# Kernel tuning notes

Measured on AMD Instinct MI355X. Metric: run time of the kernel, lower is better.

## Reference

```python
import jax, jax.numpy as jnp
import numpy as np

HEIGHT = 32
SIGMA = 2.0
NUM_NEGATIVE = 4096
N, C = 32, 512
L = HEIGHT * HEIGHT


def _grid_weight(height: int, sigma: float) -> jnp.ndarray:
    # distance_weights: pairwise Euclidean distance between grid points
    ii, jj = np.meshgrid(np.arange(height), np.arange(height), indexing='ij')
    coords = np.stack([ii.ravel(), jj.ravel()], axis=1).astype(np.float32)  # [L, 2]
    d2 = ((coords[:, None, :] - coords[None, :, :]) ** 2).sum(-1)  # squared dist [L, L]
    w = -(0.5 / sigma ** 2) * d2
    np.fill_diagonal(w, -np.inf)
    return jax.nn.softmax(jnp.asarray(w, dtype=jnp.float32), axis=1)


def setup_inputs() -> dict:
    key = jax.random.key(0)
    k1, k2 = jax.random.split(key)
    embedding = jax.random.normal(k1, (N, L, C), dtype=jnp.float32)
    weight = _grid_weight(HEIGHT, SIGMA)  # [L, L] softmax-normalized grid kernel
    neg_indices = jax.random.randint(k2, (NUM_NEGATIVE,), 0, N * L, dtype=jnp.int64)
    return {"embedding": embedding, "weight": weight, "neg_indices": neg_indices}


def reference(embedding, weight, neg_indices):
    n, l, c = embedding.shape
    # F.normalize(dim=-1), eps=1e-12
    norm = jnp.maximum(jnp.linalg.norm(embedding, axis=-1, keepdims=True), 1e-12)
    e = embedding / norm  # [N, L, C]
    # target = weight @ e  (broadcast over batch)
    target = jnp.einsum('kl,nlc->nkc', weight, e)  # [N, L, C]
    sim_pos = jnp.sum(e * target, axis=-1)  # [N, L]
    flat = e.reshape(-1, c)  # [N*L, C]
    negatives = flat[neg_indices]  # [M, C]
    sim_neg = jnp.einsum('nlc,mc->nlm', e, negatives)  # [N, L, M]
    logits = jnp.concatenate([sim_pos[..., None], sim_neg], axis=2).reshape(n * l, 1 + neg_indices.shape[0])
    # CrossEntropyLoss with target class 0, mean reduction
    loss = -jnp.mean(jax.nn.log_softmax(logits, axis=-1)[:, 0])
    return loss
```

## Files before the change

kernel.cpp:

```cpp
#include <hip/hip_runtime.h>
#include <hip/hip_bf16.h>
#include <stdint.h>

#define L_DIM 1024
#define C_DIM 512
#define CB4 256
#define N_BATCH 32
#define M_NEG 4096
#define NROWS (N_BATCH * L_DIM)

typedef float f32x4 __attribute__((ext_vector_type(4)));
typedef int i32x4 __attribute__((ext_vector_type(4)));
typedef int i32x8 __attribute__((ext_vector_type(8)));

#define E4_SCALE 32.0f
#define MX_SCALE 122
#define FMT_FP4 4

template <int GOFF>
__device__ __forceinline__ void gl_lds16(const uint8_t* g, uint8_t* l) {
  __builtin_amdgcn_global_load_lds(
      (const __attribute__((address_space(1))) void*)g,
      (__attribute__((address_space(3))) void*)l, 16, GOFF, 0);
}

__device__ __forceinline__ uint32_t fp4_enc(float x) {
  const uint32_t s = (__float_as_uint(x) >> 31) << 3;
  const float a = fabsf(x);
  uint32_t c;
  c = a < 0.25f ? 0u
    : a < 0.75f ? 1u
    : a < 1.25f ? 2u
    : a < 1.75f ? 3u
    : a < 2.5f  ? 4u
    : a < 3.5f  ? 5u
    : a < 5.0f  ? 6u : 7u;
  return s | c;
}

__device__ __forceinline__ i32x8 fp4_op(i32x4 d) {
  return __builtin_shufflevector(d, d, 0, 1, 2, 3, -1, -1, -1, -1);
}

__device__ __forceinline__ int swz(int row) { return (row >> 1) & 3; }

#define WAITK(n) asm volatile("s_waitcnt vmcnt(" #n ")\n\ts_barrier" ::: "memory")
#define BARRIER() asm volatile("s_barrier" ::: "memory")

__global__ __launch_bounds__(256) void k_normalize(const float* __restrict__ emb,
                                                   uint8_t* __restrict__ out,
                                                   float* __restrict__ zerobuf,
                                                   float* __restrict__ loss_out) {
  if (blockIdx.x < 256) zerobuf[blockIdx.x * 256 + threadIdx.x] = 0.0f;
  if (blockIdx.x == 0 && threadIdx.x == 0) loss_out[0] = 0.0f;
  const int lane = threadIdx.x & 63;
  const int wave = threadIdx.x >> 6;
  const long row = (long)blockIdx.x * 4 + wave;
  const float4* src = (const float4*)(emb + row * C_DIM);
  float4 v0 = src[2 * lane];
  float4 v1 = src[2 * lane + 1];
  float ss = v0.x * v0.x + v0.y * v0.y + v0.z * v0.z + v0.w * v0.w +
             v1.x * v1.x + v1.y * v1.y + v1.z * v1.z + v1.w * v1.w;
#pragma unroll
  for (int off = 1; off < 64; off <<= 1) ss += __shfl_xor(ss, off, 64);
  const float s = E4_SCALE / fmaxf(sqrtf(ss), 1e-12f);
  uint32_t pk = fp4_enc(v0.x * s)        | (fp4_enc(v0.y * s) << 4) |
                (fp4_enc(v0.z * s) << 8) | (fp4_enc(v0.w * s) << 12) |
                (fp4_enc(v1.x * s) << 16)| (fp4_enc(v1.y * s) << 20) |
                (fp4_enc(v1.z * s) << 24)| (fp4_enc(v1.w * s) << 28);
  ((uint32_t*)(out + row * CB4))[lane] = pk;
}

__global__ __launch_bounds__(256, 4) void k_gemm_fused(
    const uint8_t* __restrict__ E4, const int* __restrict__ idx,
    const float* __restrict__ W, float* __restrict__ rowsum,
    float* __restrict__ simpos) {
  __shared__ __align__(16) unsigned char smem_raw[32768];
  uint8_t* sA = (uint8_t*)smem_raw;
  uint8_t* sB = sA + 16384;

  const int tid = threadIdx.x;
  const int lane = tid & 63;
  const int wave = tid >> 6;
  const int wm = wave >> 1, wn = wave & 1;
  const int q = lane >> 4, c16 = lane & 15;

  const int bid = blockIdx.x;
  const bool is0 = bid >= 2048;
  long rowBase, colBase, n = 0;
  if (is0) {
    const int t = bid - 2048;
    const int xcd = t & 7, slot = t >> 3;
    rowBase = (long)(xcd * 32 + (slot & 31)) * 128;
    colBase = (long)(slot >> 5) * 128;
  } else {
    const int xcd = bid & 7, slot = bid >> 3;
    n = xcd * 4 + (slot & 3);
    const int inner = slot >> 2;
    rowBase = (long)(inner & 7) * 128;
    colBase = (long)(inner >> 3) * 128;
  }
  const long aBase = is0 ? rowBase : n * L_DIM + rowBase;

  const uint8_t* pA[2];
  const uint8_t* pB[2];
#pragma unroll
  for (int r = 0; r < 2; ++r) {
    const int c = r * 256 + tid;
    const int rw = c >> 2, cb = c & 3;
    pA[r] = E4 + (aBase + rw) * CB4 + (cb ^ swz(rw)) * 16;
    const long bRow = is0 ? (long)idx[colBase + rw] : n * L_DIM + colBase + rw;
    pB[r] = E4 + bRow * CB4 + (cb ^ swz(rw)) * 16;
  }

  int ldsB[4], ldsA[4];
#pragma unroll
  for (int j = 0; j < 4; ++j) {
    const int rowB = wn * 64 + j * 16 + c16;
    ldsB[j] = rowB * 64 + (q ^ swz(rowB)) * 16;
    const int rowA = wm * 64 + j * 16 + c16;
    ldsA[j] = rowA * 64 + (q ^ swz(rowA)) * 16;
  }

  f32x4 acc[4][4] = {};

  auto kcompute = [&](int kofs) {
    i32x8 bfr[4];
#pragma unroll
    for (int j = 0; j < 4; ++j)
      bfr[j] = fp4_op(*(const i32x4*)(sB + kofs + ldsB[j]));
#pragma unroll
    for (int i = 0; i < 4; ++i) {
      i32x8 af = fp4_op(*(const i32x4*)(sA + kofs + ldsA[i]));
#pragma unroll
      for (int j = 0; j < 4; ++j)
        acc[i][j] = __builtin_amdgcn_mfma_scale_f32_16x16x128_f8f6f4(
            af, bfr[j], acc[i][j], FMT_FP4, FMT_FP4,
            0, MX_SCALE, 0, MX_SCALE);
    }
  };

  gl_lds16<0>(pA[0], sA + tid * 16);
  gl_lds16<0>(pA[1], sA + (256 + tid) * 16);
  gl_lds16<0>(pB[0], sB + tid * 16);
  gl_lds16<0>(pB[1], sB + (256 + tid) * 16);
  gl_lds16<64>(pA[0], sA + 8192 + tid * 16);
  gl_lds16<64>(pA[1], sA + 8192 + (256 + tid) * 16);
  gl_lds16<64>(pB[0], sB + 8192 + tid * 16);
  gl_lds16<64>(pB[1], sB + 8192 + (256 + tid) * 16);

  WAITK(4);
  kcompute(0);
  BARRIER();
  gl_lds16<128>(pA[0], sA + tid * 16);
  gl_lds16<128>(pA[1], sA + (256 + tid) * 16);
  gl_lds16<128>(pB[0], sB + tid * 16);
  gl_lds16<128>(pB[1], sB + (256 + tid) * 16);
  WAITK(4);
  kcompute(8192);
  BARRIER();
  gl_lds16<192>(pA[0], sA + 8192 + tid * 16);
  gl_lds16<192>(pA[1], sA + 8192 + (256 + tid) * 16);
  gl_lds16<192>(pB[0], sB + 8192 + tid * 16);
  gl_lds16<192>(pB[1], sB + 8192 + (256 + tid) * 16);
  WAITK(4);
  kcompute(0);
  WAITK(0);
  kcompute(8192);

  if (is0) {
#pragma unroll
    for (int i = 0; i < 4; ++i)
#pragma unroll
      for (int r = 0; r < 4; ++r) {
        float s = __expf(acc[i][0][r]) + __expf(acc[i][1][r]) +
                  __expf(acc[i][2][r]) + __expf(acc[i][3][r]);
        s += __shfl_xor(s, 1, 64);
        s += __shfl_xor(s, 2, 64);
        s += __shfl_xor(s, 4, 64);
        s += __shfl_xor(s, 8, 64);
        if (c16 == 0)
          atomicAdd(&rowsum[rowBase + wm * 64 + i * 16 + q * 4 + r], s);
      }
  } else {
    const float* Wp = W + (rowBase + wm * 64) * L_DIM + colBase + wn * 64 + c16;
#pragma unroll
    for (int i = 0; i < 4; ++i)
#pragma unroll
      for (int r = 0; r < 4; ++r) {
        const float* wrow = Wp + (i * 16 + q * 4 + r) * L_DIM;
        float v = acc[i][0][r] * wrow[0]  + acc[i][1][r] * wrow[16] +
                  acc[i][2][r] * wrow[32] + acc[i][3][r] * wrow[48];
        v += __shfl_xor(v, 1, 64);
        v += __shfl_xor(v, 2, 64);
        v += __shfl_xor(v, 4, 64);
        v += __shfl_xor(v, 8, 64);
        if (c16 == 0)
          atomicAdd(&simpos[n * L_DIM + rowBase + wm * 64 + i * 16 + q * 4 + r],
                    v);
      }
  }
}

__global__ __launch_bounds__(256) void k_finalize(const float* __restrict__ rowsum,
                                                  const float* __restrict__ simpos,
                                                  float* __restrict__ out) {
  const int gid = blockIdx.x * 256 + threadIdx.x;
  const float sp = simpos[gid];
  float v = __logf(rowsum[gid] + __expf(sp)) - sp;
#pragma unroll
  for (int off = 1; off < 64; off <<= 1) v += __shfl_xor(v, off, 64);
  __shared__ float ws[4];
  if ((threadIdx.x & 63) == 0) ws[threadIdx.x >> 6] = v;
  __syncthreads();
  if (threadIdx.x == 0)
    atomicAdd(out, (ws[0] + ws[1] + ws[2] + ws[3]) * (1.0f / (float)NROWS));
}

extern "C" void kernel_launch(void* const* d_in, const int* in_sizes, int n_in,
                              void* d_out, int out_size, void* d_ws, size_t ws_size,
                              hipStream_t stream) {
  const float* emb = (const float*)d_in[0];
  const float* weight = (const float*)d_in[1];
  const int* negidx = (const int*)d_in[2];
  float* out = (float*)d_out;
  char* ws = (char*)d_ws;

  uint8_t* E4 = (uint8_t*)ws;
  float* rowsum = (float*)(ws + 8388608);
  float* simpos = (float*)(ws + 8519680);

  k_normalize<<<NROWS / 4, 256, 0, stream>>>(emb, E4, rowsum, out);
  k_gemm_fused<<<10240, 256, 0, stream>>>(E4, negidx, weight, rowsum, simpos);
  k_finalize<<<NROWS / 256, 256, 0, stream>>>(rowsum, simpos, out);
}
```

Measured before the change: 185.2 us.

## Convert fused GEMM to persistent multi-tile blocks with cross-tile prefetch pipelining

Launches 1024 blocks instead of 10240, and each block walks ten 128x128 output tiles: two positive-similarity tiles followed by eight negative tiles. The global-to-LDS loads for the next tile are issued before the current tile's epilogue, so prologue and epilogue latency overlap. Row reductions now go through LDS so there is one atomic per row per tile rather than one per wave. It also raises wave priority around the MFMA sequences. In exchange it adds LDS barriers and more complex scheduling, and with fewer blocks load balance across CUs is coarser.

Measured after the change: 349.4 us. 1.89x slower.

```diff
diff --git a/kernel.cpp b/kernel.cpp
--- a/kernel.cpp
+++ b/kernel.cpp
@@ -46,6 +46,7 @@
 
 #define WAITK(n) asm volatile("s_waitcnt vmcnt(" #n ")\n\ts_barrier" ::: "memory")
 #define BARRIER() asm volatile("s_barrier" ::: "memory")
+#define LBAR() asm volatile("s_waitcnt lgkmcnt(0)\n\ts_barrier" ::: "memory")
 
 __global__ __launch_bounds__(256) void k_normalize(const float* __restrict__ emb,
                                                    uint8_t* __restrict__ out,
@@ -75,42 +76,36 @@
     const uint8_t* __restrict__ E4, const int* __restrict__ idx,
     const float* __restrict__ W, float* __restrict__ rowsum,
     float* __restrict__ simpos) {
-  __shared__ __align__(16) unsigned char smem_raw[32768];
+  __shared__ __align__(16) unsigned char smem_raw[33792];
   uint8_t* sA = (uint8_t*)smem_raw;
   uint8_t* sB = sA + 16384;
+  float* S2 = (float*)(smem_raw + 32768);
 
   const int tid = threadIdx.x;
   const int lane = tid & 63;
   const int wave = tid >> 6;
   const int wm = wave >> 1, wn = wave & 1;
   const int q = lane >> 4, c16 = lane & 15;
-
-  const int bid = blockIdx.x;
-  const bool is0 = bid >= 2048;
-  long rowBase, colBase, n = 0;
-  if (is0) {
-    const int t = bid - 2048;
-    const int xcd = t & 7, slot = t >> 3;
-    rowBase = (long)(xcd * 32 + (slot & 31)) * 128;
-    colBase = (long)(slot >> 5) * 128;
-  } else {
-    const int xcd = bid & 7, slot = bid >> 3;
-    n = xcd * 4 + (slot & 3);
-    const int inner = slot >> 2;
-    rowBase = (long)(inner & 7) * 128;
-    colBase = (long)(inner >> 3) * 128;
-  }
-  const long aBase = is0 ? rowBase : n * L_DIM + rowBase;
-
-  const uint8_t* pA[2];
-  const uint8_t* pB[2];
-#pragma unroll
-  for (int r = 0; r < 2; ++r) {
-    const int c = r * 256 + tid;
-    const int rw = c >> 2, cb = c & 3;
-    pA[r] = E4 + (aBase + rw) * CB4 + (cb ^ swz(rw)) * 16;
-    const long bRow = is0 ? (long)idx[colBase + rw] : n * L_DIM + colBase + rw;
-    pB[r] = E4 + bRow * CB4 + (cb ^ swz(rw)) * 16;
+  const int b = blockIdx.x;
+
+  const long n1   = (long)((b & 7) * 4 + ((b >> 3) & 3));
+  const long row1 = (long)((b >> 5) & 7) * 128;
+  const long col1 = (long)(b >> 8) * 128;
+  const long row0 = (long)((b & 7) * 32 + ((b >> 3) & 31)) * 128;
+  const long col0 = (long)(b >> 8) * 128;
+
+  const int rw0 = tid >> 2, rw1 = 64 + (tid >> 2), cb = tid & 3;
+  const long off0 = (long)((cb ^ swz(rw0)) * 16);
+  const long off1 = (long)((cb ^ swz(rw1)) * 16);
+  const long rowAdd0 = (long)rw0 * CB4 + off0;
+  const long rowAdd1 = (long)rw1 * CB4 + off1;
+
+  const uint8_t *pA0, *pA1, *pB0, *pB1;
+  {
+    const long aB = (n1 * L_DIM + row1) * CB4;
+    const long bB = (n1 * L_DIM + col1) * CB4;
+    pA0 = E4 + aB + rowAdd0;  pA1 = E4 + aB + rowAdd1;
+    pB0 = E4 + bB + rowAdd0;  pB1 = E4 + bB + rowAdd1;
   }
 
   int ldsB[4], ldsA[4];
@@ -124,11 +119,25 @@
 
   f32x4 acc[4][4] = {};
 
+#define ISS(GOFF, BUF) do { \
+    gl_lds16<GOFF>(pA0, sA + (BUF) + tid * 16); \
+    gl_lds16<GOFF>(pA1, sA + (BUF) + 4096 + tid * 16); \
+    gl_lds16<GOFF>(pB0, sB + (BUF) + tid * 16); \
+    gl_lds16<GOFF>(pB1, sB + (BUF) + 4096 + tid * 16); \
+  } while (0)
+
+#define ACC0() do { \
+    _Pragma("unroll") for (int _i = 0; _i < 4; ++_i) \
+    _Pragma("unroll") for (int _j = 0; _j < 4; ++_j) \
+      acc[_i][_j] = (f32x4){0.f, 0.f, 0.f, 0.f}; \
+  } while (0)
+
   auto kcompute = [&](int kofs) {
     i32x8 bfr[4];
 #pragma unroll
     for (int j = 0; j < 4; ++j)
       bfr[j] = fp4_op(*(const i32x4*)(sB + kofs + ldsB[j]));
+    __builtin_amdgcn_s_setprio(1);
 #pragma unroll
     for (int i = 0; i < 4; ++i) {
       i32x8 af = fp4_op(*(const i32x4*)(sA + kofs + ldsA[i]));
@@ -138,37 +147,10 @@
             af, bfr[j], acc[i][j], FMT_FP4, FMT_FP4,
             0, MX_SCALE, 0, MX_SCALE);
     }
+    __builtin_amdgcn_s_setprio(0);
   };
 
-  gl_lds16<0>(pA[0], sA + tid * 16);
-  gl_lds16<0>(pA[1], sA + (256 + tid) * 16);
-  gl_lds16<0>(pB[0], sB + tid * 16);
-  gl_lds16<0>(pB[1], sB + (256 + tid) * 16);
-  gl_lds16<64>(pA[0], sA + 8192 + tid * 16);
-  gl_lds16<64>(pA[1], sA + 8192 + (256 + tid) * 16);
-  gl_lds16<64>(pB[0], sB + 8192 + tid * 16);
-  gl_lds16<64>(pB[1], sB + 8192 + (256 + tid) * 16);
-
-  WAITK(4);
-  kcompute(0);
-  BARRIER();
-  gl_lds16<128>(pA[0], sA + tid * 16);
-  gl_lds16<128>(pA[1], sA + (256 + tid) * 16);
-  gl_lds16<128>(pB[0], sB + tid * 16);
-  gl_lds16<128>(pB[1], sB + (256 + tid) * 16);
-  WAITK(4);
-  kcompute(8192);
-  BARRIER();
-  gl_lds16<192>(pA[0], sA + 8192 + tid * 16);
-  gl_lds16<192>(pA[1], sA + 8192 + (256 + tid) * 16);
-  gl_lds16<192>(pB[0], sB + 8192 + tid * 16);
-  gl_lds16<192>(pB[1], sB + 8192 + (256 + tid) * 16);
-  WAITK(4);
-  kcompute(0);
-  WAITK(0);
-  kcompute(8192);
-
-  if (is0) {
+  auto epi0 = [&](long ER) {
 #pragma unroll
     for (int i = 0; i < 4; ++i)
 #pragma unroll
@@ -179,27 +161,94 @@
         s += __shfl_xor(s, 2, 64);
         s += __shfl_xor(s, 4, 64);
         s += __shfl_xor(s, 8, 64);
-        if (c16 == 0)
-          atomicAdd(&rowsum[rowBase + wm * 64 + i * 16 + q * 4 + r], s);
+        if (c16 == 0) S2[wave * 64 + i * 16 + q * 4 + r] = s;
       }
-  } else {
-    const float* Wp = W + (rowBase + wm * 64) * L_DIM + colBase + wn * 64 + c16;
+    LBAR();
+    if (tid < 128) {
+      const int base = (tid >> 6) * 128 + (tid & 63);
+      atomicAdd(&rowsum[ER + tid], S2[base] + S2[base + 64]);
+    }
+  };
+
+  auto epi1 = [&](long ER, long EC, long EN) {
+    const float* Wp = W + (ER + wm * 64) * L_DIM + EC + wn * 64 + c16;
 #pragma unroll
     for (int i = 0; i < 4; ++i)
 #pragma unroll
       for (int r = 0; r < 4; ++r) {
-        const float* wrow = Wp + (i * 16 + q * 4 + r) * L_DIM;
-        float v = acc[i][0][r] * wrow[0]  + acc[i][1][r] * wrow[16] +
-                  acc[i][2][r] * wrow[32] + acc[i][3][r] * wrow[48];
+        const float* wr = Wp + (i * 16 + q * 4 + r) * L_DIM;
+        float v = acc[i][0][r] * wr[0]  + acc[i][1][r] * wr[16] +
+                  acc[i][2][r] * wr[32] + acc[i][3][r] * wr[48];
         v += __shfl_xor(v, 1, 64);
         v += __shfl_xor(v, 2, 64);
         v += __shfl_xor(v, 4, 64);
         v += __shfl_xor(v, 8, 64);
-        if (c16 == 0)
-          atomicAdd(&simpos[n * L_DIM + rowBase + wm * 64 + i * 16 + q * 4 + r],
-                    v);
+        if (c16 == 0) S2[wave * 64 + i * 16 + q * 4 + r] = v;
       }
-  }
+    LBAR();
+    if (tid < 128) {
+      const int base = (tid >> 6) * 128 + (tid & 63);
+      atomicAdd(&simpos[EN * L_DIM + ER + tid], S2[base] + S2[base + 64]);
+    }
+  };
+
+  ISS(0, 0);
+  ISS(64, 8192);
+
+  WAITK(4); kcompute(0);    BARRIER(); ISS(128, 0);
+  WAITK(4); kcompute(8192); BARRIER(); ISS(192, 8192);
+  WAITK(4); kcompute(0);    BARRIER();
+  pB0 += 512 * CB4; pB1 += 512 * CB4;
+  ISS(0, 0);
+  WAITK(4); kcompute(8192); BARRIER(); ISS(64, 8192);
+  epi1(row1, col1, n1);
+  ACC0();
+
+  WAITK(4); kcompute(0);    BARRIER(); ISS(128, 0);
+  WAITK(4); kcompute(8192); BARRIER();
+  {
+    const int i0 = idx[col0 + rw0];
+    const int i1 = idx[col0 + rw1];
+    ISS(192, 8192);
+    WAITK(6); kcompute(0);  BARRIER();
+    pA0 = E4 + row0 * CB4 + rowAdd0;
+    pA1 = E4 + row0 * CB4 + rowAdd1;
+    pB0 = E4 + (long)i0 * CB4 + off0;
+    pB1 = E4 + (long)i1 * CB4 + off1;
+    ISS(0, 0);
+  }
+  WAITK(4); kcompute(8192); BARRIER(); ISS(64, 8192);
+  epi1(row1, col1 + 512, n1);
+  ACC0();
+
+  long nxcol = col0 + 512;
+#pragma unroll 1
+  for (int it = 0; it < 7; ++it) {
+    WAITK(4); kcompute(0);    BARRIER(); ISS(128, 0);
+    WAITK(4); kcompute(8192); BARRIER();
+    {
+      const int j0 = idx[nxcol + rw0];
+      const int j1 = idx[nxcol + rw1];
+      ISS(192, 8192);
+      WAITK(6); kcompute(0);  BARRIER();
+      pB0 = E4 + (long)j0 * CB4 + off0;
+      pB1 = E4 + (long)j1 * CB4 + off1;
+      ISS(0, 0);
+    }
+    WAITK(4); kcompute(8192); BARRIER(); ISS(64, 8192);
+    epi0(row0);
+    ACC0();
+    nxcol += 512;
+  }
+
+  WAITK(4); kcompute(0);    BARRIER(); ISS(128, 0);
+  WAITK(4); kcompute(8192); BARRIER(); ISS(192, 8192);
+  WAITK(4); kcompute(0);    BARRIER();
+  WAITK(0); kcompute(8192);
+  epi0(row0);
+
+#undef ISS
+#undef ACC0
 }
 
 __global__ __launch_bounds__(256) void k_finalize(const float* __restrict__ rowsum,
@@ -231,6 +280,6 @@
   float* simpos = (float*)(ws + 8519680);
 
   k_normalize<<<NROWS / 4, 256, 0, stream>>>(emb, E4, rowsum, out);
-  k_gemm_fused<<<10240, 256, 0, stream>>>(E4, negidx, weight, rowsum, simpos);
+  k_gemm_fused<<<1024, 256, 0, stream>>>(E4, negidx, weight, rowsum, simpos);
   k_finalize<<<NROWS / 256, 256, 0, stream>>>(rowsum, simpos, out);
 }
```
